# Kernel optimization log

Hardware: AMD Instinct MI355X
Metric: run time of the kernel (lower is better)

Reference implementation:

```python
import jax, jax.numpy as jnp
import numpy as np

N = 50000      # nodes
E = 1600000    # edges (avg degree 32)
NF = 128       # hidden_nf
L = 4          # n_layers
EA = 1         # edge_attr_nf


def setup_inputs() -> dict:
    key = jax.random.key(0)
    ks = jax.random.split(key, 10)
    return {
        "pos": jax.random.normal(ks[0], (N, 3), jnp.float32),
        "v": jax.random.normal(ks[1], (N, 3), jnp.float32),
        "edge_attr": jax.random.normal(ks[2], (E, EA), jnp.float32),
        # phi: Linear(1+EA -> NF), SiLU, Linear(NF -> 1, no bias), Tanh
        "phi_w1": jax.random.normal(ks[3], (L, 1 + EA, NF), jnp.float32) * 0.1,
        "phi_b1": jnp.zeros((L, NF), jnp.float32),
        "phi_w2": jax.random.normal(ks[4], (L, NF, 1), jnp.float32) * 0.001,
        # coord_mlp_vel: Linear(1 -> NF), SiLU, Linear(NF -> 1)
        "vel_w1": jax.random.normal(ks[5], (L, 1, NF), jnp.float32) * 0.1,
        "vel_b1": jnp.zeros((L, NF), jnp.float32),
        "vel_w2": jax.random.normal(ks[6], (L, NF, 1), jnp.float32) * 0.1,
        "vel_b2": jnp.zeros((L, 1), jnp.float32),
        "edge_index": jax.random.randint(ks[7], (2, E), 0, N, dtype=jnp.int64),
    }


def _layer(x, vel_norm, v, row, col, edge_attr,
           pw1, pb1, pw2, vw1, vb1, vw2, vb2):
    # edge model: gather endpoints, radial feature, per-edge MLP
    x_diff = x[row] - x[col]                                        # [E,3]
    radial = jnp.sqrt(jnp.sum(x_diff * x_diff, axis=1, keepdims=True))  # [E,1]
    e_in = jnp.concatenate([radial, edge_attr], axis=1)             # [E,1+EA]
    h = jax.nn.silu(e_in @ pw1 + pb1)                               # [E,NF]
    e_out = jnp.tanh(h @ pw2)                                       # [E,1]
    m = x_diff * e_out                                              # [E,3]
    # node model: segment mean over receiving node (row)
    agg = jax.ops.segment_sum(m, row, num_segments=N)               # [N,3]
    cnt = jax.ops.segment_sum(jnp.ones((row.shape[0], 1), x.dtype), row,
                              num_segments=N)                        # [N,1]
    x = x + agg / jnp.maximum(cnt, 1.0)
    # velocity term: x += v * coord_mlp_vel(||v||)
    phi_v = jax.nn.silu(vel_norm @ vw1 + vb1) @ vw2 + vb2           # [N,1]
    return x + v * phi_v


def reference(pos, v, edge_attr, phi_w1, phi_b1, phi_w2,
              vel_w1, vel_b1, vel_w2, vel_b2, edge_index):
    row, col = edge_index[0], edge_index[1]
    vel_norm = jnp.sqrt(jnp.sum(v * v, axis=1, keepdims=True))      # [N,1]
    x = pos
    for i in range(L):
        x = _layer(x, vel_norm, v, row, col, edge_attr,
                   phi_w1[i], phi_b1[i], phi_w2[i],
                   vel_w1[i], vel_b1[i], vel_w2[i], vel_b2[i])
    return x
```

## Files before the change

### kernel.cpp

```cpp
#include <hip/hip_runtime.h>
#include <hip/hip_fp16.h>

#define NF 128
#define NL 4

#define NR 128
#define RMAXF 16.0f
#define NA 32
#define AMINF -8.0f
#define ARANGE 16.0f
#define NV 512
#define VMAXF 8.0f

#define BROWS_SHIFT 7
#define BROWS 128
#define NBMAX 512
#define BCAP 4480
#define EPT 16
#define EPB 4096

__device__ __forceinline__ float fast_sigmoid(float x) {
    float z = __builtin_amdgcn_exp2f(-1.44269504f * x);
    return __builtin_amdgcn_rcpf(1.0f + z);
}
__device__ __forceinline__ float silu(float x) { return x * fast_sigmoid(x); }

__device__ __forceinline__ float fast_tanh(float x) {
    float y = fminf(fmaxf(x, -15.0f), 15.0f);
    float e2 = __builtin_amdgcn_exp2f(2.88539008f * y);
    return (e2 - 1.0f) * __builtin_amdgcn_rcpf(e2 + 1.0f);
}

__global__ __launch_bounds__(256) void setup1_kernel(
    const float* __restrict__ pw1, const float* __restrict__ pb1,
    const float* __restrict__ pw2, const float* __restrict__ vw1,
    const float* __restrict__ vb1, const float* __restrict__ vw2,
    const float* __restrict__ vb2,
    __half* __restrict__ etabh, float* __restrict__ vtab,
    int* __restrict__ counts, int* __restrict__ cursor)
{
    int t = blockIdx.x * 256 + threadIdx.x;
    if (t < NBMAX) counts[t] = 0;
    if (t == 0) *cursor = 0;

    if (t < NL * NR * NA) {
        int l = t / (NR * NA), rem = t - l * NR * NA;
        int ri = rem / NA, ai = rem - ri * NA;
        float r = ri * (RMAXF / (NR - 1));
        float a = AMINF + ai * (ARANGE / (NA - 1));
        const float* w1r = pw1 + l * 2 * NF;
        const float* w1a = w1r + NF;
        const float* b1  = pb1 + l * NF;
        const float* w2  = pw2 + l * NF;
        float acc = 0.f;
        #pragma unroll 8
        for (int k = 0; k < NF; ++k) {
            float pre = fmaf(r, w1r[k], fmaf(a, w1a[k], b1[k]));
            acc = fmaf(silu(pre), w2[k], acc);
        }
        etabh[t] = __float2half(fast_tanh(acc));
    } else if (t < NL * NR * NA + NL * NV) {
        int u = t - NL * NR * NA;
        int l = u / NV, vi = u - l * NV;
        float vn = vi * (VMAXF / (NV - 1));
        const float* w1 = vw1 + l * NF;
        const float* b1 = vb1 + l * NF;
        const float* w2 = vw2 + l * NF;
        float acc = 0.f;
        #pragma unroll 8
        for (int k = 0; k < NF; ++k) {
            float pre = fmaf(vn, w1[k], b1[k]);
            acc = fmaf(silu(pre), w2[k], acc);
        }
        vtab[u] = acc + vb2[l];
    }
}

__global__ __launch_bounds__(256) void passA_setup2_kernel(
    const int* __restrict__ row, const int* __restrict__ col,
    const float* __restrict__ ea, int* __restrict__ counts,
    unsigned int* __restrict__ coarse, int E, int gA,
    const __half* __restrict__ etabh, __half2* __restrict__ tab2,
    const float* __restrict__ pos, const float* __restrict__ v,
    const float* __restrict__ vtab,
    float4* __restrict__ x4A, float4* __restrict__ v4,
    float* __restrict__ phv, int N)
{
    int tid = threadIdx.x;
    if ((int)blockIdx.x < gA) {
        __shared__ int hist[NBMAX];
        __shared__ int base[NBMAX];
        for (int i = tid; i < NBMAX; i += 256) hist[i] = 0;
        __syncthreads();
        int e0 = blockIdx.x * EPB;
        unsigned int rec[EPT];
        int bin[EPT];
        int rank[EPT];
        #pragma unroll
        for (int k = 0; k < EPT; ++k) {
            int e = e0 + k * 256 + tid;
            bin[k] = -1;
            if (e < E) {
                int r = row[e];
                int c = col[e];
                float a = fminf(fmaxf(ea[e], AMINF), AMINF + ARANGE);
                int aq = (int)fmaf(a - AMINF, (NA - 1) / ARANGE, 0.5f);
                bin[k]  = r >> BROWS_SHIFT;
                rec[k]  = ((unsigned int)(r & (BROWS - 1)) << 25) |
                          ((unsigned int)c << 5) | (unsigned int)aq;
                rank[k] = atomicAdd(&hist[bin[k]], 1);
            }
        }
        __syncthreads();
        for (int i = tid; i < NBMAX; i += 256) {
            int h = hist[i];
            base[i] = (h > 0) ? atomicAdd(&counts[i], h) : 0;
        }
        __syncthreads();
        #pragma unroll
        for (int k = 0; k < EPT; ++k) {
            if (bin[k] >= 0) {
                int p = base[bin[k]] + rank[k];
                if (p < BCAP) coarse[(size_t)bin[k] * BCAP + p] = rec[k];
            }
        }
    } else {
        int t = ((int)blockIdx.x - gA) * 256 + tid;
        if (t < NL * NR * NA) {
            int rem = t % (NR * NA);
            int ri = rem / NA;
            int dr = (ri + 1 < NR) ? NA : 0;
            tab2[t] = __halves2half2(etabh[t], etabh[t + dr]);
        }
        if (t < N) {
            x4A[t] = make_float4(pos[t*3], pos[t*3+1], pos[t*3+2], 0.f);
            float vx = v[t*3], vy = v[t*3+1], vz = v[t*3+2];
            v4[t] = make_float4(vx, vy, vz, 0.f);
            float vn = sqrtf(vx*vx + vy*vy + vz*vz);
            float vt = fminf(vn * ((NV - 1) / VMAXF), NV - 1.0002f);
            int k0 = (int)vt; float fv = vt - (float)k0;
            #pragma unroll
            for (int l = 0; l < NL; ++l) {
                const float* vt_l = vtab + l * NV;
                phv[l * N + t] = fmaf(fv, vt_l[k0+1] - vt_l[k0], vt_l[k0]);
            }
        }
    }
}

__global__ __launch_bounds__(256) void passB_kernel(
    const unsigned int* __restrict__ coarse, const int* __restrict__ counts,
    int* __restrict__ cursor, unsigned int* __restrict__ slots,
    int2* __restrict__ sc, int N)
{
    __shared__ unsigned int recs[BCAP];
    __shared__ int hist[BROWS];
    __shared__ int excl[BROWS];
    __shared__ int cur[BROWS];
    __shared__ int cb_sh;
    int b = blockIdx.x, tid = threadIdx.x;
    int n = min(counts[b], BCAP);
    for (int i = tid; i < n; i += 256) recs[i] = coarse[(size_t)b * BCAP + i];
    if (tid < BROWS) hist[tid] = 0;
    __syncthreads();
    for (int i = tid; i < n; i += 256) atomicAdd(&hist[recs[i] >> 25], 1);
    __syncthreads();
    if (tid < BROWS) excl[tid] = (hist[tid] + 3) & ~3;
    __syncthreads();
    for (int d = 1; d < BROWS; d <<= 1) {
        int vv = 0;
        if (tid < BROWS && tid >= d) vv = excl[tid - d];
        __syncthreads();
        if (tid < BROWS) excl[tid] += vv;
        __syncthreads();
    }
    if (tid == 0) cb_sh = atomicAdd(cursor, excl[BROWS - 1]);
    __syncthreads();
    int cb = cb_sh;
    if (tid < BROWS) {
        int h  = hist[tid];
        int ha = (h + 3) & ~3;
        int e  = excl[tid] - ha;
        cur[tid] = e;
        int r = b * BROWS + tid;
        if (r < N) sc[r] = make_int2(cb + e, h);
        unsigned int saferec = ((unsigned int)min(r, N - 1) << 5);
        for (int p = h; p < ha; ++p) slots[cb + e + p] = saferec;
    }
    __syncthreads();
    for (int i = tid; i < n; i += 256) {
        unsigned int rc = recs[i];
        int p = atomicAdd(&cur[rc >> 25], 1);
        slots[cb + p] = rc & 0x01FFFFFFu;
    }
}

__global__ __launch_bounds__(256) void layer_kernel(
    const float4* __restrict__ xo, float4* __restrict__ xn4,
    float* __restrict__ xn3,
    const unsigned int* __restrict__ slots, const int2* __restrict__ sc,
    const __half2* __restrict__ tab2, const float4* __restrict__ v4,
    const float* __restrict__ phv, int n)
{
    int sub = threadIdx.x & 15;
    int r = blockIdx.x * 16 + (threadIdx.x >> 4);
    if (r >= n) return;
    int2 s = sc[r];
    int m = s.y;
    float4 xr = xo[r];
    float mx = 0.f, my = 0.f, mz = 0.f;

    for (int kb = sub * 4; kb < m; kb += 64) {
        uint4 q = *reinterpret_cast<const uint4*>(slots + s.x + kb);
        float4 xc0 = xo[(q.x >> 5) & 0x1FFFF];
        float4 xc1 = xo[(q.y >> 5) & 0x1FFFF];
        float4 xc2 = xo[(q.z >> 5) & 0x1FFFF];
        float4 xc3 = xo[(q.w >> 5) & 0x1FFFF];

        #define EDGE(REC, XC, W) do {                                        \
            float dx_ = xr.x - (XC).x, dy_ = xr.y - (XC).y, dz_ = xr.z - (XC).z; \
            float rad_ = sqrtf(dx_*dx_ + dy_*dy_ + dz_*dz_);                 \
            float rt_ = fminf(rad_ * ((NR - 1) / RMAXF), NR - 1.0002f);      \
            int i0_ = (int)rt_; float fr_ = rt_ - (float)i0_;                \
            __half2 p_ = tab2[i0_ * NA + ((REC) & 31)];                      \
            float lo_ = __low2float(p_), hi_ = __high2float(p_);             \
            float e_ = fmaf(fr_, hi_ - lo_, lo_) * (W);                      \
            mx = fmaf(dx_, e_, mx); my = fmaf(dy_, e_, my); mz = fmaf(dz_, e_, mz); \
        } while (0)

        EDGE(q.x, xc0, 1.0f);
        EDGE(q.y, xc1, (kb + 1 < m) ? 1.0f : 0.0f);
        EDGE(q.z, xc2, (kb + 2 < m) ? 1.0f : 0.0f);
        EDGE(q.w, xc3, (kb + 3 < m) ? 1.0f : 0.0f);
        #undef EDGE
    }

    #pragma unroll
    for (int d = 1; d < 16; d <<= 1) {
        mx += __shfl_xor(mx, d);
        my += __shfl_xor(my, d);
        mz += __shfl_xor(mz, d);
    }
    if (sub == 0) {
        float inv = __builtin_amdgcn_rcpf(fmaxf((float)m, 1.0f));
        float4 vv = v4[r];
        float ph = phv[r];
        float ox = fmaf(mx, inv, fmaf(vv.x, ph, xr.x));
        float oy = fmaf(my, inv, fmaf(vv.y, ph, xr.y));
        float oz = fmaf(mz, inv, fmaf(vv.z, ph, xr.z));
        if (xn3) { xn3[r*3+0] = ox; xn3[r*3+1] = oy; xn3[r*3+2] = oz; }
        else     { xn4[r] = make_float4(ox, oy, oz, 0.f); }
    }
}

extern "C" void kernel_launch(void* const* d_in, const int* in_sizes, int n_in,
                              void* d_out, int out_size, void* d_ws, size_t ws_size,
                              hipStream_t stream) {
    const float* pos = (const float*)d_in[0];
    const float* v   = (const float*)d_in[1];
    const float* ea  = (const float*)d_in[2];
    const float* pw1 = (const float*)d_in[3];
    const float* pb1 = (const float*)d_in[4];
    const float* pw2 = (const float*)d_in[5];
    const float* vw1 = (const float*)d_in[6];
    const float* vb1 = (const float*)d_in[7];
    const float* vw2 = (const float*)d_in[8];
    const float* vb2 = (const float*)d_in[9];
    const int*   ei  = (const int*)d_in[10];

    const int N = in_sizes[0] / 3;
    const int E = in_sizes[10] / 2;
    const int* row = ei;
    const int* col = ei + E;
    const int nb = (N + BROWS - 1) >> BROWS_SHIFT;

    char*   ws  = (char*)d_ws;
    float4* x4A = (float4*)ws;
    float4* x4B = x4A + N;
    float4* v4  = x4B + N;
    __half2* tab2 = (__half2*)(v4 + N);
    unsigned int* coarse = (unsigned int*)(tab2 + (size_t)NL * NR * NA);
    unsigned int* slots  = coarse + (size_t)nb * BCAP;
    int2*   sc     = (int2*)(slots + (size_t)E + 4*(size_t)N + 64);
    float*  phv    = (float*)(sc + N);
    __half* etabh  = (__half*)(phv + (size_t)NL * N);
    float*  vtab   = (float*)(etabh + (size_t)NL * NR * NA);
    int*    counts = (int*)(vtab + (size_t)NL * NV);
    int*    cursor = counts + NBMAX;

    float* x = (float*)d_out;
    dim3 blk(256);

    int t1 = NL * NR * NA + NL * NV;
    setup1_kernel<<<(t1 + 255)/256, blk, 0, stream>>>(
        pw1, pb1, pw2, vw1, vb1, vw2, vb2, etabh, vtab, counts, cursor);

    int gA  = (E + EPB - 1) / EPB;
    int t2  = (NL * NR * NA > N) ? NL * NR * NA : N;
    int gS2 = (t2 + 255) / 256;
    passA_setup2_kernel<<<gA + gS2, blk, 0, stream>>>(
        row, col, ea, counts, coarse, E, gA,
        etabh, tab2, pos, v, vtab, x4A, v4, phv, N);

    passB_kernel<<<nb, blk, 0, stream>>>(coarse, counts, cursor, slots, sc, N);

    int gR = (N + 15) / 16;
    const size_t TSZ = (size_t)NR * NA;
    layer_kernel<<<gR, blk, 0, stream>>>(x4A, x4B, nullptr, slots, sc, tab2 + 0*TSZ, v4, phv + 0*(size_t)N, N);
    layer_kernel<<<gR, blk, 0, stream>>>(x4B, x4A, nullptr, slots, sc, tab2 + 1*TSZ, v4, phv + 1*(size_t)N, N);
    layer_kernel<<<gR, blk, 0, stream>>>(x4A, x4B, nullptr, slots, sc, tab2 + 2*TSZ, v4, phv + 2*(size_t)N, N);
    layer_kernel<<<gR, blk, 0, stream>>>(x4B, nullptr, x,   slots, sc, tab2 + 3*TSZ, v4, phv + 3*(size_t)N, N);
}
```

Before: 97.07 us.

## Fold table setup into passA kernel and compute velocity MLP per node exactly

Removes the separate setup kernel. The edge-MLP lookup table pairs (r, r+1) are now computed directly inside the passA setup branch, and the velocity MLP is evaluated exactly per node instead of through a 512-entry interpolated table. Counter zeroing moves to a hipMemsetAsync. This saves one kernel launch and a dependency, but each node now runs 4×128 silu evaluations, and the memset is still a separate stream operation.

```diff
diff --git a/kernel.cpp b/kernel.cpp
--- a/kernel.cpp
+++ b/kernel.cpp
@@ -9,9 +9,6 @@
 #define NA 32
 #define AMINF -8.0f
 #define ARANGE 16.0f
-#define NV 512
-#define VMAXF 8.0f
-
 #define BROWS_SHIFT 7
 #define BROWS 128
 #define NBMAX 512
@@ -31,58 +28,16 @@
     return (e2 - 1.0f) * __builtin_amdgcn_rcpf(e2 + 1.0f);
 }
 
-__global__ __launch_bounds__(256) void setup1_kernel(
+__global__ __launch_bounds__(256) void passA_setup_kernel(
+    const int* __restrict__ row, const int* __restrict__ col,
+    const float* __restrict__ ea, int* __restrict__ counts,
+    unsigned int* __restrict__ coarse, int E, int gA,
     const float* __restrict__ pw1, const float* __restrict__ pb1,
     const float* __restrict__ pw2, const float* __restrict__ vw1,
     const float* __restrict__ vb1, const float* __restrict__ vw2,
     const float* __restrict__ vb2,
-    __half* __restrict__ etabh, float* __restrict__ vtab,
-    int* __restrict__ counts, int* __restrict__ cursor)
-{
-    int t = blockIdx.x * 256 + threadIdx.x;
-    if (t < NBMAX) counts[t] = 0;
-    if (t == 0) *cursor = 0;
-
-    if (t < NL * NR * NA) {
-        int l = t / (NR * NA), rem = t - l * NR * NA;
-        int ri = rem / NA, ai = rem - ri * NA;
-        float r = ri * (RMAXF / (NR - 1));
-        float a = AMINF + ai * (ARANGE / (NA - 1));
-        const float* w1r = pw1 + l * 2 * NF;
-        const float* w1a = w1r + NF;
-        const float* b1  = pb1 + l * NF;
-        const float* w2  = pw2 + l * NF;
-        float acc = 0.f;
-        #pragma unroll 8
-        for (int k = 0; k < NF; ++k) {
-            float pre = fmaf(r, w1r[k], fmaf(a, w1a[k], b1[k]));
-            acc = fmaf(silu(pre), w2[k], acc);
-        }
-        etabh[t] = __float2half(fast_tanh(acc));
-    } else if (t < NL * NR * NA + NL * NV) {
-        int u = t - NL * NR * NA;
-        int l = u / NV, vi = u - l * NV;
-        float vn = vi * (VMAXF / (NV - 1));
-        const float* w1 = vw1 + l * NF;
-        const float* b1 = vb1 + l * NF;
-        const float* w2 = vw2 + l * NF;
-        float acc = 0.f;
-        #pragma unroll 8
-        for (int k = 0; k < NF; ++k) {
-            float pre = fmaf(vn, w1[k], b1[k]);
-            acc = fmaf(silu(pre), w2[k], acc);
-        }
-        vtab[u] = acc + vb2[l];
-    }
-}
-
-__global__ __launch_bounds__(256) void passA_setup2_kernel(
-    const int* __restrict__ row, const int* __restrict__ col,
-    const float* __restrict__ ea, int* __restrict__ counts,
-    unsigned int* __restrict__ coarse, int E, int gA,
-    const __half* __restrict__ etabh, __half2* __restrict__ tab2,
+    __half2* __restrict__ tab2,
     const float* __restrict__ pos, const float* __restrict__ v,
-    const float* __restrict__ vtab,
     float4* __restrict__ x4A, float4* __restrict__ v4,
     float* __restrict__ phv, int N)
 {
@@ -127,22 +82,43 @@
     } else {
         int t = ((int)blockIdx.x - gA) * 256 + tid;
         if (t < NL * NR * NA) {
-            int rem = t % (NR * NA);
-            int ri = rem / NA;
-            int dr = (ri + 1 < NR) ? NA : 0;
-            tab2[t] = __halves2half2(etabh[t], etabh[t + dr]);
+            int l = t / (NR * NA), rem = t - l * NR * NA;
+            int ri = rem / NA, ai = rem - ri * NA;
+            float r0 = ri * (RMAXF / (NR - 1));
+            float r1 = min(ri + 1, NR - 1) * (RMAXF / (NR - 1));
+            float a  = AMINF + ai * (ARANGE / (NA - 1));
+            const float* w1r = pw1 + l * 2 * NF;
+            const float* w1a = w1r + NF;
+            const float* b1  = pb1 + l * NF;
+            const float* w2  = pw2 + l * NF;
+            float acc0 = 0.f, acc1 = 0.f;
+            #pragma unroll 8
+            for (int k = 0; k < NF; ++k) {
+                float ab = fmaf(a, w1a[k], b1[k]);
+                float wr = w1r[k], w2k = w2[k];
+                acc0 = fmaf(silu(fmaf(r0, wr, ab)), w2k, acc0);
+                acc1 = fmaf(silu(fmaf(r1, wr, ab)), w2k, acc1);
+            }
+            tab2[t] = __halves2half2(__float2half(fast_tanh(acc0)),
+                                     __float2half(fast_tanh(acc1)));
         }
         if (t < N) {
             x4A[t] = make_float4(pos[t*3], pos[t*3+1], pos[t*3+2], 0.f);
             float vx = v[t*3], vy = v[t*3+1], vz = v[t*3+2];
             v4[t] = make_float4(vx, vy, vz, 0.f);
             float vn = sqrtf(vx*vx + vy*vy + vz*vz);
-            float vt = fminf(vn * ((NV - 1) / VMAXF), NV - 1.0002f);
-            int k0 = (int)vt; float fv = vt - (float)k0;
             #pragma unroll
             for (int l = 0; l < NL; ++l) {
-                const float* vt_l = vtab + l * NV;
-                phv[l * N + t] = fmaf(fv, vt_l[k0+1] - vt_l[k0], vt_l[k0]);
+                const float* w1 = vw1 + l * NF;
+                const float* b1 = vb1 + l * NF;
+                const float* w2 = vw2 + l * NF;
+                float acc = 0.f;
+                #pragma unroll 8
+                for (int k = 0; k < NF; ++k) {
+                    float pre = fmaf(vn, w1[k], b1[k]);
+                    acc = fmaf(silu(pre), w2[k], acc);
+                }
+                phv[l * N + t] = acc + vb2[l];
             }
         }
     }
@@ -283,24 +259,21 @@
     unsigned int* slots  = coarse + (size_t)nb * BCAP;
     int2*   sc     = (int2*)(slots + (size_t)E + 4*(size_t)N + 64);
     float*  phv    = (float*)(sc + N);
-    __half* etabh  = (__half*)(phv + (size_t)NL * N);
-    float*  vtab   = (float*)(etabh + (size_t)NL * NR * NA);
-    int*    counts = (int*)(vtab + (size_t)NL * NV);
-    int*    cursor = counts + NBMAX;
+    int*    counts = (int*)(phv + (size_t)NL * N);
 
     float* x = (float*)d_out;
     dim3 blk(256);
 
-    int t1 = NL * NR * NA + NL * NV;
-    setup1_kernel<<<(t1 + 255)/256, blk, 0, stream>>>(
-        pw1, pb1, pw2, vw1, vb1, vw2, vb2, etabh, vtab, counts, cursor);
+    hipMemsetAsync(counts, 0, (NBMAX + 1) * sizeof(int), stream);
+    int* cursor = counts + NBMAX;
 
     int gA  = (E + EPB - 1) / EPB;
     int t2  = (NL * NR * NA > N) ? NL * NR * NA : N;
     int gS2 = (t2 + 255) / 256;
-    passA_setup2_kernel<<<gA + gS2, blk, 0, stream>>>(
+    passA_setup_kernel<<<gA + gS2, blk, 0, stream>>>(
         row, col, ea, counts, coarse, E, gA,
-        etabh, tab2, pos, v, vtab, x4A, v4, phv, N);
+        pw1, pb1, pw2, vw1, vb1, vw2, vb2,
+        tab2, pos, v, x4A, v4, phv, N);
 
     passB_kernel<<<nb, blk, 0, stream>>>(coarse, counts, cursor, slots, sc, N);
 
```

After: 111.6 us. 15.0% more time.
